# Kernel tuning notes

Hardware: AMD Instinct MI355X
Metric: run time of the kernel (lower is better)

## Reference

```python
import jax, jax.numpy as jnp
import numpy as np

N_HEAD = 16
LN_EPS = 1e-5


def setup_inputs() -> dict:
    key = jax.random.key(0)
    ks = jax.random.split(key, 12)
    B, S, D = 4, 1024, 1024
    s = 1.0 / np.sqrt(D)
    return {
        "Q": jax.random.normal(ks[0], (B, S, D), jnp.float32),
        "K": jax.random.normal(ks[1], (B, S, D), jnp.float32),
        "V": jax.random.normal(ks[2], (B, S, D), jnp.float32),
        # Linear weights stored torch-style [out, in]
        "Wq": jax.random.normal(ks[3], (D, D), jnp.float32) * s,
        "bq": jnp.zeros((D,), jnp.float32),
        "Wk": jax.random.normal(ks[4], (D, D), jnp.float32) * s,
        "bk": jnp.zeros((D,), jnp.float32),
        "Wv": jax.random.normal(ks[5], (D, D), jnp.float32) * s,
        "bv": jnp.zeros((D,), jnp.float32),
        "Wo": jax.random.normal(ks[6], (D, D), jnp.float32) * s,
        "bo": jnp.zeros((D,), jnp.float32),
        "ln_g": jnp.ones((D,), jnp.float32),
        "ln_b": jnp.zeros((D,), jnp.float32),
    }


def _layer_norm(x, g, b):
    mu = jnp.mean(x, axis=-1, keepdims=True)
    var = jnp.mean(jnp.square(x - mu), axis=-1, keepdims=True)
    return (x - mu) * jax.lax.rsqrt(var + LN_EPS) * g + b


def reference(Q, K, V, Wq, bq, Wk, bk, Wv, bv, Wo, bo, ln_g, ln_b):
    B, S, D = Q.shape
    H = N_HEAD
    dk = D // H
    # projections, split heads: [B, H, S, dk]
    q = (Q @ Wq.T + bq).reshape(B, S, H, dk).transpose(0, 2, 1, 3)
    k = (K @ Wk.T + bk).reshape(B, S, H, dk).transpose(0, 2, 1, 3)
    v = (V @ Wv.T + bv).reshape(B, S, H, dk).transpose(0, 2, 1, 3)
    scores = jnp.einsum("bhqd,bhkd->bhqk", q, k) / np.sqrt(dk)
    # NOTE: original module applies softmax twice (F.softmax then nn.Softmax)
    attn = jax.nn.softmax(jax.nn.softmax(scores, axis=-1), axis=-1)
    ctx = jnp.einsum("bhqk,bhkd->bhqd", attn, v)  # [B, H, S, dk]
    ctx = ctx.transpose(0, 2, 1, 3).reshape(B, S, D)
    out = ctx @ Wo.T + bo
    return _layer_norm(out + Q, ln_g, ln_b)
```

## Files before the change

### kernel.cpp

```cpp
#include <hip/hip_runtime.h>
#include <cstdint>
#include <cstddef>


typedef unsigned short ushort_t;
typedef __attribute__((ext_vector_type(8))) short bf16x8;
typedef __attribute__((ext_vector_type(8))) unsigned short us8;
typedef __attribute__((ext_vector_type(4))) unsigned short us4;
typedef __attribute__((ext_vector_type(4))) float f32x4;

#define MFMA16(a, b, c) __builtin_amdgcn_mfma_f32_16x16x32_bf16((a), (b), (c), 0, 0, 0)

__device__ __forceinline__ float b2f(ushort_t u) {
  union { unsigned int i; float f; } x; x.i = ((unsigned int)u) << 16; return x.f;
}
__device__ __forceinline__ ushort_t f2b(float f) {
  union { unsigned int i; float f; } x; x.f = f;
  unsigned int r = (x.i + 0x7FFFu + ((x.i >> 16) & 1u)) >> 16;
  return (ushort_t)r;
}
__device__ __forceinline__ us8 cvt8(float4 a, float4 b) {
  us8 r;
  r[0] = f2b(a.x); r[1] = f2b(a.y); r[2] = f2b(a.z); r[3] = f2b(a.w);
  r[4] = f2b(b.x); r[5] = f2b(b.y); r[6] = f2b(b.z); r[7] = f2b(b.w);
  return r;
}

__global__ __launch_bounds__(256, 8) void cvt_kernel(
    const float* __restrict__ src, ushort_t* __restrict__ dst, int n) {
  const int i = (blockIdx.x * 256 + threadIdx.x) * 8;
  if (i < n) {
    const float4 a = *(const float4*)(src + i);
    const float4 b = *(const float4*)(src + i + 4);
    *(us8*)(dst + i) = cvt8(a, b);
  }
}

__global__ __launch_bounds__(256, 3) void qkv_proj_kernel(
    const float* __restrict__ Qin, const float* __restrict__ Kin,
    const float* __restrict__ Vin,
    const float* __restrict__ Wq, const float* __restrict__ Wk,
    const float* __restrict__ Wv,
    const float* __restrict__ bq, const float* __restrict__ bk,
    const float* __restrict__ bv,
    ushort_t* __restrict__ qb, ushort_t* __restrict__ kb,
    ushort_t* __restrict__ vb) {
  __shared__ __align__(16) ushort_t Asl[128 * 32];
  __shared__ __align__(16) ushort_t Bsl[128 * 32];
  const float* A; const float* B; const float* bias; float scale;
  if (blockIdx.z == 0)      { A = Qin; B = Wq; bias = bq; scale = 0.125f; }
  else if (blockIdx.z == 1) { A = Kin; B = Wk; bias = bk; scale = 1.0f; }
  else                      { A = Vin; B = Wv; bias = bv; scale = 1.0f; }
  const int m0 = blockIdx.y * 128, n0 = blockIdx.x * 128;
  const int tid = threadIdx.x;
  const int wave = tid >> 6, lane = tid & 63;
  const int l15 = lane & 15, quad = lane >> 4;
  const int wm = (wave & 1) * 64, wn = (wave >> 1) * 64;

  const int r0 = tid >> 2, c0 = (tid & 3) * 8;
  const int r1 = (tid + 256) >> 2, c1 = c0;

  const float* Ap0 = A + (size_t)(m0 + r0) * 1024 + c0;
  const float* Ap1 = A + (size_t)(m0 + r1) * 1024 + c1;
  const float* Bp0 = B + (size_t)(n0 + r0) * 1024 + c0;
  const float* Bp1 = B + (size_t)(n0 + r1) * 1024 + c1;

  float4 a0l, a0h, a1l, a1h, b0l, b0h, b1l, b1h;
  a0l = *(const float4*)(Ap0); a0h = *(const float4*)(Ap0 + 4);
  a1l = *(const float4*)(Ap1); a1h = *(const float4*)(Ap1 + 4);
  b0l = *(const float4*)(Bp0); b0h = *(const float4*)(Bp0 + 4);
  b1l = *(const float4*)(Bp1); b1h = *(const float4*)(Bp1 + 4);

  f32x4 acc[4][4] = {};
  for (int k0 = 0; k0 < 1024; k0 += 32) {
    __syncthreads();
    *(us8*)(Asl + r0 * 32 + c0) = cvt8(a0l, a0h);
    *(us8*)(Asl + r1 * 32 + c1) = cvt8(a1l, a1h);
    *(us8*)(Bsl + r0 * 32 + c0) = cvt8(b0l, b0h);
    *(us8*)(Bsl + r1 * 32 + c1) = cvt8(b1l, b1h);
    __syncthreads();
    if (k0 + 32 < 1024) {
      const int k = k0 + 32;
      a0l = *(const float4*)(Ap0 + k); a0h = *(const float4*)(Ap0 + k + 4);
      a1l = *(const float4*)(Ap1 + k); a1h = *(const float4*)(Ap1 + k + 4);
      b0l = *(const float4*)(Bp0 + k); b0h = *(const float4*)(Bp0 + k + 4);
      b1l = *(const float4*)(Bp1 + k); b1h = *(const float4*)(Bp1 + k + 4);
    }
    bf16x8 af[4], bfr[4];
#pragma unroll
    for (int s = 0; s < 4; ++s) {
      af[s]  = *(const bf16x8*)(Asl + (wm + s * 16 + l15) * 32 + quad * 8);
      bfr[s] = *(const bf16x8*)(Bsl + (wn + s * 16 + l15) * 32 + quad * 8);
    }
#pragma unroll
    for (int ms = 0; ms < 4; ++ms)
#pragma unroll
      for (int ns = 0; ns < 4; ++ns)
        acc[ms][ns] = MFMA16(af[ms], bfr[ns], acc[ms][ns]);
  }

  if (blockIdx.z != 2) {
    ushort_t* outp = (blockIdx.z == 0) ? qb : kb;
#pragma unroll
    for (int ns = 0; ns < 4; ++ns) {
      const int col = n0 + wn + ns * 16 + l15;
      const float bv_ = bias[col];
#pragma unroll
      for (int ms = 0; ms < 4; ++ms) {
        const int rowb = m0 + wm + ms * 16 + quad * 4;
#pragma unroll
        for (int r = 0; r < 4; ++r) {
          outp[(size_t)(rowb + r) * 1024 + col] =
              f2b((acc[ms][ns][r] + bv_) * scale);
        }
      }
    }
  } else {
#pragma unroll
    for (int ns = 0; ns < 4; ++ns) {
      const int col = n0 + wn + ns * 16 + l15;
      const float bv_ = bias[col];
      const int h = col >> 6, d = col & 63;
#pragma unroll
      for (int ms = 0; ms < 4; ++ms) {
        const int i0 = m0 + wm + ms * 16 + quad * 4;
        const int b = i0 >> 10, s0 = i0 & 1023;
        us4 pack;
#pragma unroll
        for (int r = 0; r < 4; ++r) pack[r] = f2b(acc[ms][ns][r] + bv_);
        *(us4*)(vb + ((size_t)(b * 16 + h) * 64 + d) * 1024 + s0) = pack;
      }
    }
  }
}

__global__ __launch_bounds__(256, 4) void attn_kernel(
    const ushort_t* __restrict__ qb, const ushort_t* __restrict__ kb,
    const ushort_t* __restrict__ vb, ushort_t* __restrict__ ctx) {
  __shared__ __align__(16) ushort_t Qs[64 * 72];
  __shared__ __align__(16) ushort_t Ks[64 * 72];
  __shared__ __align__(16) ushort_t Vt[64 * 72];
  __shared__ __align__(16) ushort_t Ps[4][16 * 68];

  const int tid = threadIdx.x, wave = tid >> 6, lane = tid & 63;
  const int l15 = lane & 15, quad = lane >> 4;
  const int bh = blockIdx.y;
  const int b = bh >> 4, h = bh & 15;
  const int q0 = blockIdx.x * 64;
  const ushort_t* qg = qb + ((size_t)b << 20) + h * 64;
  const ushort_t* kg = kb + ((size_t)b << 20) + h * 64;
  const ushort_t* vg = vb + ((size_t)bh << 16);

  const int kr0 = tid >> 3, kc0 = (tid & 7) * 8;
  const int kr1 = (tid + 256) >> 3, kc1 = kc0;

  *(us8*)(Qs + kr0 * 72 + kc0) = *(const us8*)(qg + (size_t)(q0 + kr0) * 1024 + kc0);
  *(us8*)(Qs + kr1 * 72 + kc1) = *(const us8*)(qg + (size_t)(q0 + kr1) * 1024 + kc1);

  float z1[4] = {0.f, 0.f, 0.f, 0.f};
  us8 rk0 = *(const us8*)(kg + (size_t)kr0 * 1024 + kc0);
  us8 rk1 = *(const us8*)(kg + (size_t)kr1 * 1024 + kc1);
  for (int kt = 0; kt < 16; ++kt) {
    __syncthreads();
    *(us8*)(Ks + kr0 * 72 + kc0) = rk0;
    *(us8*)(Ks + kr1 * 72 + kc1) = rk1;
    __syncthreads();
    if (kt < 15) {
      rk0 = *(const us8*)(kg + (size_t)((kt + 1) * 64 + kr0) * 1024 + kc0);
      rk1 = *(const us8*)(kg + (size_t)((kt + 1) * 64 + kr1) * 1024 + kc1);
    }
    f32x4 sc[4] = {};
#pragma unroll
    for (int kk = 0; kk < 2; ++kk) {
      const bf16x8 aq = *(const bf16x8*)(Qs + (wave * 16 + l15) * 72 + kk * 32 + quad * 8);
#pragma unroll
      for (int ns = 0; ns < 4; ++ns) {
        const bf16x8 bk_ = *(const bf16x8*)(Ks + (ns * 16 + l15) * 72 + kk * 32 + quad * 8);
        sc[ns] = MFMA16(aq, bk_, sc[ns]);
      }
    }
#pragma unroll
    for (int ns = 0; ns < 4; ++ns)
#pragma unroll
      for (int r = 0; r < 4; ++r) z1[r] += __expf(sc[ns][r]);
  }
  float iz1[4];
#pragma unroll
  for (int r = 0; r < 4; ++r) {
    float s = z1[r];
#pragma unroll
    for (int off = 1; off < 16; off <<= 1) s += __shfl_xor(s, off, 64);
    iz1[r] = 1.0f / s;
  }

  f32x4 oac[4] = {};
  float z2[4] = {0.f, 0.f, 0.f, 0.f};
  rk0 = *(const us8*)(kg + (size_t)kr0 * 1024 + kc0);
  rk1 = *(const us8*)(kg + (size_t)kr1 * 1024 + kc1);
  us8 rv0 = *(const us8*)(vg + (size_t)kr0 * 1024 + kc0);
  us8 rv1 = *(const us8*)(vg + (size_t)kr1 * 1024 + kc1);
  for (int kt = 0; kt < 16; ++kt) {
    __syncthreads();
    *(us8*)(Ks + kr0 * 72 + kc0) = rk0;
    *(us8*)(Ks + kr1 * 72 + kc1) = rk1;
    *(us8*)(Vt + kr0 * 72 + kc0) = rv0;
    *(us8*)(Vt + kr1 * 72 + kc1) = rv1;
    __syncthreads();
    if (kt < 15) {
      rk0 = *(const us8*)(kg + (size_t)((kt + 1) * 64 + kr0) * 1024 + kc0);
      rk1 = *(const us8*)(kg + (size_t)((kt + 1) * 64 + kr1) * 1024 + kc1);
      rv0 = *(const us8*)(vg + (size_t)kr0 * 1024 + (kt + 1) * 64 + kc0);
      rv1 = *(const us8*)(vg + (size_t)kr1 * 1024 + (kt + 1) * 64 + kc1);
    }
    f32x4 sc[4] = {};
#pragma unroll
    for (int kk = 0; kk < 2; ++kk) {
      const bf16x8 aq = *(const bf16x8*)(Qs + (wave * 16 + l15) * 72 + kk * 32 + quad * 8);
#pragma unroll
      for (int ns = 0; ns < 4; ++ns) {
        const bf16x8 bk_ = *(const bf16x8*)(Ks + (ns * 16 + l15) * 72 + kk * 32 + quad * 8);
        sc[ns] = MFMA16(aq, bk_, sc[ns]);
      }
    }
#pragma unroll
    for (int ns = 0; ns < 4; ++ns)
#pragma unroll
      for (int r = 0; r < 4; ++r) {
        const float p1 = __expf(sc[ns][r]) * iz1[r];
        const float e2 = __expf(p1);
        z2[r] += e2;
        Ps[wave][(quad * 4 + r) * 68 + ns * 16 + l15] = f2b(e2);
      }
    __asm__ __volatile__("s_waitcnt lgkmcnt(0)" ::: "memory");
#pragma unroll
    for (int kk = 0; kk < 2; ++kk) {
      const ushort_t* pp = &Ps[wave][l15 * 68 + kk * 32 + quad * 8];
      union { us4 hseg[2]; bf16x8 v; } u;
      u.hseg[0] = *(const us4*)pp;
      u.hseg[1] = *(const us4*)(pp + 4);
      const bf16x8 ap = u.v;
#pragma unroll
      for (int ns2 = 0; ns2 < 4; ++ns2) {
        const bf16x8 bv_ = *(const bf16x8*)(Vt + (ns2 * 16 + l15) * 72 + kk * 32 + quad * 8);
        oac[ns2] = MFMA16(ap, bv_, oac[ns2]);
      }
    }
  }

#pragma unroll
  for (int r = 0; r < 4; ++r) {
    float s = z2[r];
#pragma unroll
    for (int off = 1; off < 16; off <<= 1) s += __shfl_xor(s, off, 64);
    z2[r] = s;
  }
#pragma unroll
  for (int ns2 = 0; ns2 < 4; ++ns2) {
    const int d = ns2 * 16 + l15;
#pragma unroll
    for (int r = 0; r < 4; ++r) {
      const int s = q0 + wave * 16 + quad * 4 + r;
      ctx[((size_t)(b * 1024 + s)) * 1024 + h * 64 + d] = f2b(oac[ns2][r] / z2[r]);
    }
  }
}

__global__ __launch_bounds__(256, 4) void out_proj_kernel(
    const ushort_t* __restrict__ ctxp, const ushort_t* __restrict__ wo,
    const float* __restrict__ bo, float* __restrict__ pre) {
  __shared__ __align__(16) ushort_t Asl[64 * 32];
  __shared__ __align__(16) ushort_t Bsl[128 * 32];
  const int tid = threadIdx.x;
  const int wave = tid >> 6, lane = tid & 63;
  const int l15 = lane & 15, quad = lane >> 4;
  const int m0 = blockIdx.y * 64, n0 = blockIdx.x * 128;
  const int wn = wave * 32;

  const int ra = tid >> 2, ca = (tid & 3) * 8;
  const int rb0 = tid >> 2, cb0 = ca;
  const int rb1 = (tid + 256) >> 2, cb1 = ca;

  us8 va = *(const us8*)(ctxp + (size_t)(m0 + ra) * 1024 + ca);
  us8 vb0 = *(const us8*)(wo + (size_t)(n0 + rb0) * 1024 + cb0);
  us8 vb1 = *(const us8*)(wo + (size_t)(n0 + rb1) * 1024 + cb1);

  f32x4 acc[4][2] = {};
  for (int k0 = 0; k0 < 1024; k0 += 32) {
    __syncthreads();
    *(us8*)(Asl + ra * 32 + ca) = va;
    *(us8*)(Bsl + rb0 * 32 + cb0) = vb0;
    *(us8*)(Bsl + rb1 * 32 + cb1) = vb1;
    __syncthreads();
    if (k0 + 32 < 1024) {
      const int k = k0 + 32;
      va  = *(const us8*)(ctxp + (size_t)(m0 + ra) * 1024 + k + ca);
      vb0 = *(const us8*)(wo + (size_t)(n0 + rb0) * 1024 + k + cb0);
      vb1 = *(const us8*)(wo + (size_t)(n0 + rb1) * 1024 + k + cb1);
    }
    bf16x8 af[4], bfr[2];
#pragma unroll
    for (int s = 0; s < 4; ++s)
      af[s] = *(const bf16x8*)(Asl + (s * 16 + l15) * 32 + quad * 8);
#pragma unroll
    for (int s = 0; s < 2; ++s)
      bfr[s] = *(const bf16x8*)(Bsl + (wn + s * 16 + l15) * 32 + quad * 8);
#pragma unroll
    for (int ms = 0; ms < 4; ++ms)
#pragma unroll
      for (int ns = 0; ns < 2; ++ns)
        acc[ms][ns] = MFMA16(af[ms], bfr[ns], acc[ms][ns]);
  }

#pragma unroll
  for (int ns = 0; ns < 2; ++ns) {
    const int col = n0 + wn + ns * 16 + l15;
    const float bv_ = bo[col];
#pragma unroll
    for (int ms = 0; ms < 4; ++ms) {
      const int rowb = m0 + ms * 16 + quad * 4;
#pragma unroll
      for (int r = 0; r < 4; ++r) {
        pre[(size_t)(rowb + r) * 1024 + col] = acc[ms][ns][r] + bv_;
      }
    }
  }
}

__global__ __launch_bounds__(256, 4) void ln_kernel(
    const float* __restrict__ pre, const float* __restrict__ Q,
    const float* __restrict__ g, const float* __restrict__ bta,
    float* __restrict__ out) {
  const int row = blockIdx.x;
  const int tid = threadIdx.x;
  const size_t base = (size_t)row * 1024 + tid * 4;
  const float4 p4 = *(const float4*)(pre + base);
  const float4 q4 = *(const float4*)(Q + base);
  float v[4] = {p4.x + q4.x, p4.y + q4.y, p4.z + q4.z, p4.w + q4.w};
  float s1 = v[0] + v[1] + v[2] + v[3];
  float s2 = v[0]*v[0] + v[1]*v[1] + v[2]*v[2] + v[3]*v[3];
#pragma unroll
  for (int off = 1; off < 64; off <<= 1) {
    s1 += __shfl_xor(s1, off, 64);
    s2 += __shfl_xor(s2, off, 64);
  }
  __shared__ float r1[4], r2[4];
  const int wave = tid >> 6, lane = tid & 63;
  if (lane == 0) { r1[wave] = s1; r2[wave] = s2; }
  __syncthreads();
  const float t1 = r1[0] + r1[1] + r1[2] + r1[3];
  const float t2 = r2[0] + r2[1] + r2[2] + r2[3];
  const float mu = t1 * (1.0f / 1024.0f);
  const float var = t2 * (1.0f / 1024.0f) - mu * mu;
  const float inv = rsqrtf(var + 1e-5f);
  const int c0 = tid * 4;
#pragma unroll
  for (int j = 0; j < 4; ++j) {
    const int c = c0 + j;
    out[(size_t)row * 1024 + c] = (v[j] - mu) * inv * g[c] + bta[c];
  }
}

extern "C" void kernel_launch(void* const* d_in, const int* in_sizes, int n_in,
                              void* d_out, int out_size, void* d_ws, size_t ws_size,
                              hipStream_t stream) {
  const float* Q  = (const float*)d_in[0];
  const float* K  = (const float*)d_in[1];
  const float* V  = (const float*)d_in[2];
  const float* Wq = (const float*)d_in[3];
  const float* bq = (const float*)d_in[4];
  const float* Wk = (const float*)d_in[5];
  const float* bk = (const float*)d_in[6];
  const float* Wv = (const float*)d_in[7];
  const float* bv = (const float*)d_in[8];
  const float* Wo = (const float*)d_in[9];
  const float* bo = (const float*)d_in[10];
  const float* lg = (const float*)d_in[11];
  const float* lb = (const float*)d_in[12];

  char* ws = (char*)d_ws;
  ushort_t* qb  = (ushort_t*)(ws);
  ushort_t* kb  = (ushort_t*)(ws + ((size_t)8  << 20));
  ushort_t* vb  = (ushort_t*)(ws + ((size_t)16 << 20));
  float*    pre = (float*)(ws);
  ushort_t* wo_bf = (ushort_t*)d_out;
  ushort_t* ctx = (ushort_t*)d_out + 4194304;
  float*    out = (float*)d_out;

  cvt_kernel<<<dim3(512), 256, 0, stream>>>(Wo, wo_bf, 1048576);
  qkv_proj_kernel<<<dim3(8, 32, 3), 256, 0, stream>>>(Q, K, V, Wq, Wk, Wv,
                                                      bq, bk, bv, qb, kb, vb);
  attn_kernel<<<dim3(16, 64), 256, 0, stream>>>(qb, kb, vb, ctx);
  out_proj_kernel<<<dim3(8, 64), 256, 0, stream>>>(ctx, wo_bf, bo, pre);
  ln_kernel<<<dim3(4096), 256, 0, stream>>>(pre, Q, lg, lb, out);
}
```

Baseline: 264.7 us.

## Pre-convert all weights to bf16, shrink QKV tile, store out-proj result in bf16

A single conversion kernel now turns Wq, Wk, Wv and Wo into bf16 up front, so the QKV projection loads bf16 weights instead of converting fp32 weights inside every tile loop. The QKV GEMM tile drops from 128x128 to 64x128, with a higher occupancy hint and twice as many blocks. The output-projection intermediate is stored in bf16 and widened again in the layernorm kernel, halving that round-trip traffic. The costs are a smaller per-block reuse of the weight tile and extra rounding of the pre-layernorm activations.

```diff
diff --git a/kernel.cpp b/kernel.cpp
--- a/kernel.cpp
+++ b/kernel.cpp
@@ -26,88 +26,86 @@
   return r;
 }
 
-__global__ __launch_bounds__(256, 8) void cvt_kernel(
-    const float* __restrict__ src, ushort_t* __restrict__ dst, int n) {
+__global__ __launch_bounds__(256, 8) void cvt4_kernel(
+    const float* __restrict__ w0, const float* __restrict__ w1,
+    const float* __restrict__ w2, const float* __restrict__ w3,
+    ushort_t* __restrict__ dst) {
+  const int which = blockIdx.y;
+  const float* src = (which == 0) ? w0 : (which == 1) ? w1 : (which == 2) ? w2 : w3;
   const int i = (blockIdx.x * 256 + threadIdx.x) * 8;
-  if (i < n) {
-    const float4 a = *(const float4*)(src + i);
-    const float4 b = *(const float4*)(src + i + 4);
-    *(us8*)(dst + i) = cvt8(a, b);
-  }
-}
-
-__global__ __launch_bounds__(256, 3) void qkv_proj_kernel(
+  const float4 a = *(const float4*)(src + i);
+  const float4 b = *(const float4*)(src + i + 4);
+  *(us8*)(dst + (size_t)which * 1048576 + i) = cvt8(a, b);
+}
+
+__global__ __launch_bounds__(256, 6) void qkv_proj_kernel(
     const float* __restrict__ Qin, const float* __restrict__ Kin,
     const float* __restrict__ Vin,
-    const float* __restrict__ Wq, const float* __restrict__ Wk,
-    const float* __restrict__ Wv,
+    const ushort_t* __restrict__ wq, const ushort_t* __restrict__ wk,
+    const ushort_t* __restrict__ wv,
     const float* __restrict__ bq, const float* __restrict__ bk,
     const float* __restrict__ bv,
     ushort_t* __restrict__ qb, ushort_t* __restrict__ kb,
     ushort_t* __restrict__ vb) {
-  __shared__ __align__(16) ushort_t Asl[128 * 32];
+  __shared__ __align__(16) ushort_t Asl[64 * 32];
   __shared__ __align__(16) ushort_t Bsl[128 * 32];
-  const float* A; const float* B; const float* bias; float scale;
-  if (blockIdx.z == 0)      { A = Qin; B = Wq; bias = bq; scale = 0.125f; }
-  else if (blockIdx.z == 1) { A = Kin; B = Wk; bias = bk; scale = 1.0f; }
-  else                      { A = Vin; B = Wv; bias = bv; scale = 1.0f; }
-  const int m0 = blockIdx.y * 128, n0 = blockIdx.x * 128;
+  const float* A; const ushort_t* W; const float* bias; float scale;
+  if (blockIdx.z == 0)      { A = Qin; W = wq; bias = bq; scale = 0.125f; }
+  else if (blockIdx.z == 1) { A = Kin; W = wk; bias = bk; scale = 1.0f; }
+  else                      { A = Vin; W = wv; bias = bv; scale = 1.0f; }
+  const int m0 = blockIdx.y * 64, n0 = blockIdx.x * 128;
   const int tid = threadIdx.x;
   const int wave = tid >> 6, lane = tid & 63;
   const int l15 = lane & 15, quad = lane >> 4;
-  const int wm = (wave & 1) * 64, wn = (wave >> 1) * 64;
-
-  const int r0 = tid >> 2, c0 = (tid & 3) * 8;
-  const int r1 = (tid + 256) >> 2, c1 = c0;
-
-  const float* Ap0 = A + (size_t)(m0 + r0) * 1024 + c0;
-  const float* Ap1 = A + (size_t)(m0 + r1) * 1024 + c1;
-  const float* Bp0 = B + (size_t)(n0 + r0) * 1024 + c0;
-  const float* Bp1 = B + (size_t)(n0 + r1) * 1024 + c1;
-
-  float4 a0l, a0h, a1l, a1h, b0l, b0h, b1l, b1h;
-  a0l = *(const float4*)(Ap0); a0h = *(const float4*)(Ap0 + 4);
-  a1l = *(const float4*)(Ap1); a1h = *(const float4*)(Ap1 + 4);
-  b0l = *(const float4*)(Bp0); b0h = *(const float4*)(Bp0 + 4);
-  b1l = *(const float4*)(Bp1); b1h = *(const float4*)(Bp1 + 4);
-
-  f32x4 acc[4][4] = {};
+  const int wn = wave * 32;
+
+  const int ra = tid >> 2, ca = (tid & 3) * 8;
+  const int rb1 = (tid + 256) >> 2;
+
+  const float* Ap = A + (size_t)(m0 + ra) * 1024 + ca;
+  const ushort_t* Bp0 = W + (size_t)(n0 + ra) * 1024 + ca;
+  const ushort_t* Bp1 = W + (size_t)(n0 + rb1) * 1024 + ca;
+
+  float4 al = *(const float4*)(Ap), ah = *(const float4*)(Ap + 4);
+  us8 rb0v = *(const us8*)(Bp0);
+  us8 rb1v = *(const us8*)(Bp1);
+
+  f32x4 acc[4][2] = {};
   for (int k0 = 0; k0 < 1024; k0 += 32) {
     __syncthreads();
-    *(us8*)(Asl + r0 * 32 + c0) = cvt8(a0l, a0h);
-    *(us8*)(Asl + r1 * 32 + c1) = cvt8(a1l, a1h);
-    *(us8*)(Bsl + r0 * 32 + c0) = cvt8(b0l, b0h);
-    *(us8*)(Bsl + r1 * 32 + c1) = cvt8(b1l, b1h);
+    *(us8*)(Asl + ra * 32 + ca) = cvt8(al, ah);
+    *(us8*)(Bsl + ra * 32 + ca) = rb0v;
+    *(us8*)(Bsl + rb1 * 32 + ca) = rb1v;
     __syncthreads();
     if (k0 + 32 < 1024) {
       const int k = k0 + 32;
-      a0l = *(const float4*)(Ap0 + k); a0h = *(const float4*)(Ap0 + k + 4);
-      a1l = *(const float4*)(Ap1 + k); a1h = *(const float4*)(Ap1 + k + 4);
-      b0l = *(const float4*)(Bp0 + k); b0h = *(const float4*)(Bp0 + k + 4);
-      b1l = *(const float4*)(Bp1 + k); b1h = *(const float4*)(Bp1 + k + 4);
-    }
-    bf16x8 af[4], bfr[4];
-#pragma unroll
-    for (int s = 0; s < 4; ++s) {
-      af[s]  = *(const bf16x8*)(Asl + (wm + s * 16 + l15) * 32 + quad * 8);
+      al = *(const float4*)(Ap + k); ah = *(const float4*)(Ap + k + 4);
+      rb0v = *(const us8*)(Bp0 + k);
+      rb1v = *(const us8*)(Bp1 + k);
+    }
+    bf16x8 af[4], bfr[2];
+#pragma unroll
+    for (int s = 0; s < 4; ++s)
+      af[s] = *(const bf16x8*)(Asl + (s * 16 + l15) * 32 + quad * 8);
+#pragma unroll
+    for (int s = 0; s < 2; ++s)
       bfr[s] = *(const bf16x8*)(Bsl + (wn + s * 16 + l15) * 32 + quad * 8);
-    }
 #pragma unroll
     for (int ms = 0; ms < 4; ++ms)
 #pragma unroll
-      for (int ns = 0; ns < 4; ++ns)
+      for (int ns = 0; ns < 2; ++ns)
         acc[ms][ns] = MFMA16(af[ms], bfr[ns], acc[ms][ns]);
   }
 
   if (blockIdx.z != 2) {
     ushort_t* outp = (blockIdx.z == 0) ? qb : kb;
 #pragma unroll
-    for (int ns = 0; ns < 4; ++ns) {
+    for (int ns = 0; ns < 2; ++ns) {
       const int col = n0 + wn + ns * 16 + l15;
       const float bv_ = bias[col];
 #pragma unroll
       for (int ms = 0; ms < 4; ++ms) {
-        const int rowb = m0 + wm + ms * 16 + quad * 4;
+        const int rowb = m0 + ms * 16 + quad * 4;
 #pragma unroll
         for (int r = 0; r < 4; ++r) {
           outp[(size_t)(rowb + r) * 1024 + col] =
@@ -117,13 +115,13 @@
     }
   } else {
 #pragma unroll
-    for (int ns = 0; ns < 4; ++ns) {
+    for (int ns = 0; ns < 2; ++ns) {
       const int col = n0 + wn + ns * 16 + l15;
       const float bv_ = bias[col];
       const int h = col >> 6, d = col & 63;
 #pragma unroll
       for (int ms = 0; ms < 4; ++ms) {
-        const int i0 = m0 + wm + ms * 16 + quad * 4;
+        const int i0 = m0 + ms * 16 + quad * 4;
         const int b = i0 >> 10, s0 = i0 & 1023;
         us4 pack;
 #pragma unroll
@@ -267,7 +265,7 @@
 
 __global__ __launch_bounds__(256, 4) void out_proj_kernel(
     const ushort_t* __restrict__ ctxp, const ushort_t* __restrict__ wo,
-    const float* __restrict__ bo, float* __restrict__ pre) {
+    const float* __restrict__ bo, ushort_t* __restrict__ pre) {
   __shared__ __align__(16) ushort_t Asl[64 * 32];
   __shared__ __align__(16) ushort_t Bsl[128 * 32];
   const int tid = threadIdx.x;
@@ -277,25 +275,24 @@
   const int wn = wave * 32;
 
   const int ra = tid >> 2, ca = (tid & 3) * 8;
-  const int rb0 = tid >> 2, cb0 = ca;
-  const int rb1 = (tid + 256) >> 2, cb1 = ca;
+  const int rb1 = (tid + 256) >> 2;
 
   us8 va = *(const us8*)(ctxp + (size_t)(m0 + ra) * 1024 + ca);
-  us8 vb0 = *(const us8*)(wo + (size_t)(n0 + rb0) * 1024 + cb0);
-  us8 vb1 = *(const us8*)(wo + (size_t)(n0 + rb1) * 1024 + cb1);
+  us8 vb0 = *(const us8*)(wo + (size_t)(n0 + ra) * 1024 + ca);
+  us8 vb1 = *(const us8*)(wo + (size_t)(n0 + rb1) * 1024 + ca);
 
   f32x4 acc[4][2] = {};
   for (int k0 = 0; k0 < 1024; k0 += 32) {
     __syncthreads();
     *(us8*)(Asl + ra * 32 + ca) = va;
-    *(us8*)(Bsl + rb0 * 32 + cb0) = vb0;
-    *(us8*)(Bsl + rb1 * 32 + cb1) = vb1;
+    *(us8*)(Bsl + ra * 32 + ca) = vb0;
+    *(us8*)(Bsl + rb1 * 32 + ca) = vb1;
     __syncthreads();
     if (k0 + 32 < 1024) {
       const int k = k0 + 32;
       va  = *(const us8*)(ctxp + (size_t)(m0 + ra) * 1024 + k + ca);
-      vb0 = *(const us8*)(wo + (size_t)(n0 + rb0) * 1024 + k + cb0);
-      vb1 = *(const us8*)(wo + (size_t)(n0 + rb1) * 1024 + k + cb1);
+      vb0 = *(const us8*)(wo + (size_t)(n0 + ra) * 1024 + k + ca);
+      vb1 = *(const us8*)(wo + (size_t)(n0 + rb1) * 1024 + k + ca);
     }
     bf16x8 af[4], bfr[2];
 #pragma unroll
@@ -320,22 +317,23 @@
       const int rowb = m0 + ms * 16 + quad * 4;
 #pragma unroll
       for (int r = 0; r < 4; ++r) {
-        pre[(size_t)(rowb + r) * 1024 + col] = acc[ms][ns][r] + bv_;
+        pre[(size_t)(rowb + r) * 1024 + col] = f2b(acc[ms][ns][r] + bv_);
       }
     }
   }
 }
 
 __global__ __launch_bounds__(256, 4) void ln_kernel(
-    const float* __restrict__ pre, const float* __restrict__ Q,
+    const ushort_t* __restrict__ pre, const float* __restrict__ Q,
     const float* __restrict__ g, const float* __restrict__ bta,
     float* __restrict__ out) {
   const int row = blockIdx.x;
   const int tid = threadIdx.x;
   const size_t base = (size_t)row * 1024 + tid * 4;
-  const float4 p4 = *(const float4*)(pre + base);
+  const ushort4 p4 = *(const ushort4*)(pre + base);
   const float4 q4 = *(const float4*)(Q + base);
-  float v[4] = {p4.x + q4.x, p4.y + q4.y, p4.z + q4.z, p4.w + q4.w};
+  float v[4] = {b2f(p4.x) + q4.x, b2f(p4.y) + q4.y,
+                b2f(p4.z) + q4.z, b2f(p4.w) + q4.w};
   float s1 = v[0] + v[1] + v[2] + v[3];
   float s2 = v[0]*v[0] + v[1]*v[1] + v[2]*v[2] + v[3]*v[3];
 #pragma unroll
@@ -381,13 +379,18 @@
   ushort_t* qb  = (ushort_t*)(ws);
   ushort_t* kb  = (ushort_t*)(ws + ((size_t)8  << 20));
   ushort_t* vb  = (ushort_t*)(ws + ((size_t)16 << 20));
-  float*    pre = (float*)(ws);
-  ushort_t* wo_bf = (ushort_t*)d_out;
-  ushort_t* ctx = (ushort_t*)d_out + 4194304;
-  float*    out = (float*)d_out;
-
-  cvt_kernel<<<dim3(512), 256, 0, stream>>>(Wo, wo_bf, 1048576);
-  qkv_proj_kernel<<<dim3(8, 32, 3), 256, 0, stream>>>(Q, K, V, Wq, Wk, Wv,
+  ushort_t* pre = (ushort_t*)(ws);
+
+  ushort_t* dptr  = (ushort_t*)d_out;
+  ushort_t* wo_bf = dptr;
+  ushort_t* wq_bf = dptr + 1048576;
+  ushort_t* wk_bf = dptr + 2097152;
+  ushort_t* wv_bf = dptr + 3145728;
+  ushort_t* ctx   = dptr + 4194304;
+  float*    out   = (float*)d_out;
+
+  cvt4_kernel<<<dim3(512, 4), 256, 0, stream>>>(Wo, Wq, Wk, Wv, dptr);
+  qkv_proj_kernel<<<dim3(8, 64, 3), 256, 0, stream>>>(Q, K, V, wq_bf, wk_bf, wv_bf,
                                                       bq, bk, bv, qb, kb, vb);
   attn_kernel<<<dim3(16, 64), 256, 0, stream>>>(qb, kb, vb, ctx);
   out_proj_kernel<<<dim3(8, 64), 256, 0, stream>>>(ctx, wo_bf, bo, pre);
```

New measurement: 267.6 us. Within noise of the previous version (+1.1%).
